# Kernel tuning notes

Measured on AMD Instinct MI355X. Metric: run time of the kernel, lower is better.

## Reference

```python
import jax, jax.numpy as jnp
import numpy as np

B1, B2, D = 8192, 8192, 128


def _cdist(d1, d2):
    # L2 distance matrix via the |a|^2 + |b|^2 - 2ab expansion (GEMM-dominant).
    d1_sq = jnp.sum(d1 * d1, axis=1, keepdims=True)          # (B1, 1)
    d2_sq = jnp.sum(d2 * d2, axis=1, keepdims=True)          # (B2, 1)
    dm = d1_sq + d2_sq.T - 2.0 * (d1 @ d2.T)                 # (B1, B2)
    return jnp.sqrt(jnp.clip(dm, 0.0))


def setup_inputs() -> dict:
    key = jax.random.key(0)
    k1, k2 = jax.random.split(key)
    desc1 = jax.random.normal(k1, (B1, D), dtype=jnp.float32)
    desc2 = jax.random.normal(k2, (B2, D), dtype=jnp.float32)
    return {"desc1": desc1, "desc2": desc2}


def reference(desc1, desc2):
    # DescriptorMatcher(match_mode='nn'): nearest neighbor in desc2 for each desc1.
    dm = _cdist(desc1, desc2)                                # (B1, B2)
    idxs_in_2 = jnp.argmin(dm, axis=1)                       # (B1,)
    match_dists = jnp.take_along_axis(dm, idxs_in_2[:, None], axis=1)  # (B1, 1)
    idxs_in_1 = jnp.arange(dm.shape[0], dtype=jnp.int64 if jax.config.jax_enable_x64 else jnp.int32)
    matches_idxs = jnp.stack([idxs_in_1, idxs_in_2.astype(idxs_in_1.dtype)], axis=1)  # (B1, 2)
    return match_dists, matches_idxs
```

## Files before the change

kernel.cpp:

```cpp
#include <hip/hip_runtime.h>
#include <cstdint>

#define NB1 8192
#define NB2 8192
#define DDIM 128
#define KROW 256
#define NSTEP 12

using half8   = __attribute__((ext_vector_type(8))) _Float16;
using half4   = __attribute__((ext_vector_type(4))) _Float16;
using float4v = __attribute__((ext_vector_type(4))) float;

typedef __attribute__((address_space(3))) void       lds_void;
typedef const __attribute__((address_space(1))) void glb_void;

__device__ inline unsigned long long packkey(float v, int j) {
  unsigned u = __float_as_uint(v);
  u = (u & 0x80000000u) ? ~u : (u | 0x80000000u);
  return ((unsigned long long)u << 32) | (unsigned)j;
}

__device__ __forceinline__ int a_src(int kt) { return (kt < 8) ? kt : kt - 8; }
__device__ __forceinline__ int b_src(int kt) { return (kt < 4) ? kt : kt - 4; }

__global__ __launch_bounds__(256) void convert_kernel(
    const float* __restrict__ d1, const float* __restrict__ d2,
    _Float16* __restrict__ A2, _Float16* __restrict__ B2,
    float* __restrict__ asq, float* __restrict__ bsq,
    unsigned long long* __restrict__ packed) {
  int gid  = blockIdx.x * 256 + threadIdx.x;
  int wv   = gid >> 6;
  int lane = gid & 63;
  int rowc = 2 * wv + (lane >> 5);
  bool isA = rowc < NB1;
  const float* src = isA ? d1 : d2;
  int row = isA ? rowc : rowc - NB1;
  int k4  = (lane & 31) * 4;

  float4 v = *(const float4*)&src[row * DDIM + k4];
  _Float16 h0 = (_Float16)v.x, h1 = (_Float16)v.y;
  _Float16 h2 = (_Float16)v.z, h3 = (_Float16)v.w;
  half4 hh = {h0, h1, h2, h3};
  half4 ll = {(_Float16)(v.x - (float)h0), (_Float16)(v.y - (float)h1),
              (_Float16)(v.z - (float)h2), (_Float16)(v.w - (float)h3)};

  _Float16* dst = (isA ? A2 : B2) + (size_t)row * KROW;
  *(half4*)&dst[k4]       = hh;
  *(half4*)&dst[128 + k4] = ll;

  float s = v.x * v.x + v.y * v.y + v.z * v.z + v.w * v.w;
  #pragma unroll
  for (int off = 16; off > 0; off >>= 1) s += __shfl_xor(s, off, 64);
  if ((lane & 31) == 0) (isA ? asq : bsq)[row] = s;

  if (gid < NB1) packed[gid] = 0xFFFFFFFFFFFFFFFFull;
}

__global__ __launch_bounds__(512, 2) void mfma_match_kernel(
    const _Float16* __restrict__ A2, const _Float16* __restrict__ B2,
    const float* __restrict__ bsq, unsigned long long* __restrict__ packed) {
  __shared__ unsigned long long smem[16384];
  _Float16* S = (_Float16*)smem;

  const int t    = threadIdx.x;
  const int lane = t & 63;
  const int wid  = t >> 6;
  const int wm   = wid >> 1;
  const int wn   = wid & 1;
  const int lx   = lane & 15, q = lane >> 4;

  const int id  = blockIdx.x;
  const int xcd = id & 7, kk = id >> 3;
  const int bx = (xcd & 1) * 16 + (kk & 15);
  const int by = (xcd >> 1) * 8 + (kk >> 4);
  const int row0 = bx * 256, col0 = by * 256;

  const int rstg  = t >> 2;
  const int cslot = t & 3;

  float4v acc[4][8];
  #pragma unroll
  for (int m = 0; m < 4; ++m)
    #pragma unroll
    for (int c = 0; c < 8; ++c) acc[m][c] = (float4v){0.f, 0.f, 0.f, 0.f};

  const int jc0 = col0 + wn * 128 + lx;
  float bq[8];
  #pragma unroll
  for (int c = 0; c < 8; ++c) bq[c] = bsq[jc0 + 16 * c];

  auto stage = [&](int kt, int buf) {
    const int koA = a_src(kt) * 32, koB = b_src(kt) * 32;
    #pragma unroll
    for (int call = 0; call < 2; ++call) {
      const int R  = call * 128 + rstg;
      const int cc = (cslot - (R >> 1)) & 3;
      const _Float16* ga = A2 + (size_t)(row0 + R) * KROW + koA + cc * 8;
      __builtin_amdgcn_global_load_lds((glb_void*)ga,
          (lds_void*)(S + buf * 16384 + call * 4096 + wid * 512), 16, 0, 0);
      const _Float16* gb = B2 + (size_t)(col0 + R) * KROW + koB + cc * 8;
      __builtin_amdgcn_global_load_lds((glb_void*)gb,
          (lds_void*)(S + buf * 16384 + 8192 + call * 4096 + wid * 512), 16, 0, 0);
    }
  };

  const int sw = ((q + (lx >> 1)) & 3) * 8;

  auto compute = [&](int buf) {
    const _Float16* Ab = S + buf * 16384;
    const _Float16* Bb = Ab + 8192;
    half8 af[4], bf[8];
    #pragma unroll
    for (int m = 0; m < 4; ++m)
      af[m] = *(const half8*)&Ab[(wm * 64 + 16 * m + lx) * 32 + sw];
    #pragma unroll
    for (int c = 0; c < 8; ++c)
      bf[c] = *(const half8*)&Bb[(wn * 128 + 16 * c + lx) * 32 + sw];
    __builtin_amdgcn_s_setprio(1);
    #pragma unroll
    for (int m = 0; m < 4; ++m)
      #pragma unroll
      for (int c = 0; c < 8; ++c)
        acc[m][c] = __builtin_amdgcn_mfma_f32_16x16x32_f16(
            af[m], bf[c], acc[m][c], 0, 0, 0);
    __builtin_amdgcn_s_setprio(0);
  };

  stage(0, 0); stage(1, 1); stage(2, 2);

#define STEP(K, N)                                                    \
  do {                                                                \
    asm volatile("s_waitcnt vmcnt(" #N ")" ::: "memory");             \
    __builtin_amdgcn_s_barrier();                                     \
    asm volatile("" ::: "memory");                                    \
    if constexpr ((K) + 3 < NSTEP) stage((K) + 3, ((K) + 3) & 3);     \
    compute((K) & 3);                                                 \
  } while (0)

  STEP(0, 8);  STEP(1, 8);  STEP(2, 8);  STEP(3, 8);
  STEP(4, 8);  STEP(5, 8);  STEP(6, 8);  STEP(7, 8);
  STEP(8, 8);  STEP(9, 8);  STEP(10, 4); STEP(11, 0);
#undef STEP

  __syncthreads();
  #pragma unroll
  for (int m = 0; m < 4; ++m) {
    #pragma unroll
    for (int reg = 0; reg < 4; ++reg) {
      float bv = 1e30f; int bj = 0;
      #pragma unroll
      for (int c = 0; c < 8; ++c) {
        float val = fmaf(-2.f, acc[m][c][reg], bq[c]);
        if (val < bv) { bv = val; bj = jc0 + 16 * c; }
      }
      const int mrow = wm * 64 + 16 * m + 4 * q + reg;
      smem[mrow * 33 + wn * 16 + lx] = packkey(bv, bj);
    }
  }
  __syncthreads();
  if (t < 256) {
    unsigned long long best = ~0ull;
    #pragma unroll
    for (int c = 0; c < 32; ++c) {
      unsigned long long kx = smem[t * 33 + ((2 * t + c) & 31)];
      if (kx < best) best = kx;
    }
    atomicMin(&packed[row0 + t], best);
  }
}

__global__ __launch_bounds__(256) void out_kernel(
    const unsigned long long* __restrict__ packed,
    const float* __restrict__ asq, float* __restrict__ out) {
  int r = blockIdx.x * 256 + threadIdx.x;
  unsigned long long best = packed[r];
  unsigned u = (unsigned)(best >> 32);
  u = (u & 0x80000000u) ? (u & 0x7fffffffu) : ~u;
  float val  = __uint_as_float(u);
  float dist = sqrtf(fmaxf(asq[r] + val, 0.f));
  int j = (int)(unsigned)(best & 0xffffffffu);
  out[r]               = dist;
  out[NB1 + 2 * r]     = (float)r;
  out[NB1 + 2 * r + 1] = (float)j;
}

extern "C" void kernel_launch(void* const* d_in, const int* in_sizes, int n_in,
                              void* d_out, int out_size, void* d_ws, size_t ws_size,
                              hipStream_t stream) {
  const float* d1 = (const float*)d_in[0];
  const float* d2 = (const float*)d_in[1];
  float* out = (float*)d_out;

  char* w = (char*)d_ws;
  float* asq = (float*)w;
  float* bsq = (float*)(w + 32768);
  _Float16* A2 = (_Float16*)(w + 65536);
  _Float16* B2 = (_Float16*)(w + 65536 + 4194304);
  unsigned long long* packed =
      (unsigned long long*)(w + 65536 + 2 * 4194304);

  convert_kernel<<<(NB1 + NB2) / 8, 256, 0, stream>>>(
      d1, d2, A2, B2, asq, bsq, packed);

  mfma_match_kernel<<<(NB1 / 256) * (NB2 / 256), 512, 0, stream>>>(
      A2, B2, bsq, packed);

  out_kernel<<<NB1 / 256, 256, 0, stream>>>(packed, asq, out);
}
```

Measured before the change: 117.8 us.

## Double-buffer LDS fragment reads into registers to overlap with MFMA

Splits the per-step compute into an LDS-read phase and an MFMA phase. It keeps two register sets of A/B fragments so the next K-step's fragments load while the current step's MFMAs run. The vmcnt waits are retuned to this one-step-ahead schedule. The bsq column-norm loads move to the epilogue to cut live registers during the main loop. A plain load now guards the atomicMin so rows that cannot improve skip the atomic. The extra fragment registers raise VGPR pressure under the 512x2 launch bound, which could cause spills or lower occupancy.

```diff
diff --git a/kernel.cpp b/kernel.cpp
--- a/kernel.cpp
+++ b/kernel.cpp
@@ -84,11 +84,6 @@
     #pragma unroll
     for (int c = 0; c < 8; ++c) acc[m][c] = (float4v){0.f, 0.f, 0.f, 0.f};
 
-  const int jc0 = col0 + wn * 128 + lx;
-  float bq[8];
-  #pragma unroll
-  for (int c = 0; c < 8; ++c) bq[c] = bsq[jc0 + 16 * c];
-
   auto stage = [&](int kt, int buf) {
     const int koA = a_src(kt) * 32, koB = b_src(kt) * 32;
     #pragma unroll
@@ -106,16 +101,18 @@
 
   const int sw = ((q + (lx >> 1)) & 3) * 8;
 
-  auto compute = [&](int buf) {
+  auto rd = [&](int buf, half8 (&af)[4], half8 (&bf)[8]) {
     const _Float16* Ab = S + buf * 16384;
     const _Float16* Bb = Ab + 8192;
-    half8 af[4], bf[8];
     #pragma unroll
     for (int m = 0; m < 4; ++m)
       af[m] = *(const half8*)&Ab[(wm * 64 + 16 * m + lx) * 32 + sw];
     #pragma unroll
     for (int c = 0; c < 8; ++c)
       bf[c] = *(const half8*)&Bb[(wn * 128 + 16 * c + lx) * 32 + sw];
+  };
+
+  auto mm = [&](half8 (&af)[4], half8 (&bf)[8]) {
     __builtin_amdgcn_s_setprio(1);
     #pragma unroll
     for (int m = 0; m < 4; ++m)
@@ -126,23 +123,44 @@
     __builtin_amdgcn_s_setprio(0);
   };
 
+  half8 afA[4], bfA[8], afB[4], bfB[8];
+
   stage(0, 0); stage(1, 1); stage(2, 2);
-
-#define STEP(K, N)                                                    \
+  asm volatile("s_waitcnt vmcnt(8)" ::: "memory");
+  __builtin_amdgcn_s_barrier();
+  asm volatile("" ::: "memory");
+  rd(0, afA, bfA);
+
+#define STEP(K, NV, MSET, RSET, DOST, DORD)                           \
   do {                                                                \
-    asm volatile("s_waitcnt vmcnt(" #N ")" ::: "memory");             \
+    asm volatile("s_waitcnt vmcnt(" #NV ")" ::: "memory");            \
     __builtin_amdgcn_s_barrier();                                     \
     asm volatile("" ::: "memory");                                    \
-    if constexpr ((K) + 3 < NSTEP) stage((K) + 3, ((K) + 3) & 3);     \
-    compute((K) & 3);                                                 \
+    if constexpr (DOST) stage((K) + 3, ((K) + 3) & 3);                \
+    if constexpr (DORD) rd(((K) + 1) & 3, af##RSET, bf##RSET);        \
+    mm(af##MSET, bf##MSET);                                           \
   } while (0)
 
-  STEP(0, 8);  STEP(1, 8);  STEP(2, 8);  STEP(3, 8);
-  STEP(4, 8);  STEP(5, 8);  STEP(6, 8);  STEP(7, 8);
-  STEP(8, 8);  STEP(9, 8);  STEP(10, 4); STEP(11, 0);
+  STEP(0, 4, A, B, true, true);
+  STEP(1, 4, B, A, true, true);
+  STEP(2, 4, A, B, true, true);
+  STEP(3, 4, B, A, true, true);
+  STEP(4, 4, A, B, true, true);
+  STEP(5, 4, B, A, true, true);
+  STEP(6, 4, A, B, true, true);
+  STEP(7, 4, B, A, true, true);
+  STEP(8, 4, A, B, true, true);
+  STEP(9, 4, B, A, false, true);
+  STEP(10, 0, A, B, false, true);
 #undef STEP
+  mm(afB, bfB);
 
   __syncthreads();
+  const int jc0 = col0 + wn * 128 + lx;
+  float bq[8];
+  #pragma unroll
+  for (int c = 0; c < 8; ++c) bq[c] = bsq[jc0 + 16 * c];
+
   #pragma unroll
   for (int m = 0; m < 4; ++m) {
     #pragma unroll
@@ -165,7 +183,8 @@
       unsigned long long kx = smem[t * 33 + ((2 * t + c) & 31)];
       if (kx < best) best = kx;
     }
-    atomicMin(&packed[row0 + t], best);
+    unsigned long long cur = packed[row0 + t];
+    if (best < cur) atomicMin(&packed[row0 + t], best);
   }
 }
 
```

After: 140.3 us. +19.1%, slower.

## Restructure MFMA match kernel into 2x4 wave grid with phased double-buffer pipeline

Applied to the files above, without the earlier changes.

The GEMM main loop is rebuilt. Waves now sit in a 2x4 grid, each owning a 128x64 output sub-tile instead of 64x128. Global-to-LDS staging moves from a 4-slot single-k-step ring to two 64KB buffers, each holding two k-slices, and each tile is split into four phases that interleave LDS reads, async prefetch and 16-MFMA batches with barriers between them. The epilogue adds a shuffle-based partial min, and the final atomicMin is skipped when the existing value is already smaller. The goal is better overlap of memory and compute and fewer LDS fragment reads per MFMA, at the cost of more barriers and more complex wait-count bookkeeping.

```diff
diff --git a/kernel.cpp b/kernel.cpp
--- a/kernel.cpp
+++ b/kernel.cpp
@@ -5,7 +5,6 @@
 #define NB2 8192
 #define DDIM 128
 #define KROW 256
-#define NSTEP 12
 
 using half8   = __attribute__((ext_vector_type(8))) _Float16;
 using half4   = __attribute__((ext_vector_type(4))) _Float16;
@@ -19,9 +18,6 @@
   u = (u & 0x80000000u) ? ~u : (u | 0x80000000u);
   return ((unsigned long long)u << 32) | (unsigned)j;
 }
-
-__device__ __forceinline__ int a_src(int kt) { return (kt < 8) ? kt : kt - 8; }
-__device__ __forceinline__ int b_src(int kt) { return (kt < 4) ? kt : kt - 4; }
 
 __global__ __launch_bounds__(256) void convert_kernel(
     const float* __restrict__ d1, const float* __restrict__ d2,
@@ -60,14 +56,16 @@
     const _Float16* __restrict__ A2, const _Float16* __restrict__ B2,
     const float* __restrict__ bsq, unsigned long long* __restrict__ packed) {
   __shared__ unsigned long long smem[16384];
-  _Float16* S = (_Float16*)smem;
+  _Float16* S  = (_Float16*)smem;
+  char*     Sb = (char*)smem;
 
   const int t    = threadIdx.x;
   const int lane = t & 63;
   const int wid  = t >> 6;
-  const int wm   = wid >> 1;
-  const int wn   = wid & 1;
+  const int wm   = wid >> 2;
+  const int wn   = wid & 3;
   const int lx   = lane & 15, q = lane >> 4;
+  const int sw   = ((q + (lx >> 1)) & 3) * 8;
 
   const int id  = blockIdx.x;
   const int xcd = id & 7, kk = id >> 3;
@@ -75,86 +73,129 @@
   const int by = (xcd >> 1) * 8 + (kk >> 4);
   const int row0 = bx * 256, col0 = by * 256;
 
-  const int rstg  = t >> 2;
-  const int cslot = t & 3;
-
-  float4v acc[4][8];
-  #pragma unroll
-  for (int m = 0; m < 4; ++m)
-    #pragma unroll
-    for (int c = 0; c < 8; ++c) acc[m][c] = (float4v){0.f, 0.f, 0.f, 0.f};
-
-  const int jc0 = col0 + wn * 128 + lx;
-  float bq[8];
-  #pragma unroll
-  for (int c = 0; c < 8; ++c) bq[c] = bsq[jc0 + 16 * c];
-
-  auto stage = [&](int kt, int buf) {
-    const int koA = a_src(kt) * 32, koB = b_src(kt) * 32;
-    #pragma unroll
-    for (int call = 0; call < 2; ++call) {
-      const int R  = call * 128 + rstg;
-      const int cc = (cslot - (R >> 1)) & 3;
-      const _Float16* ga = A2 + (size_t)(row0 + R) * KROW + koA + cc * 8;
-      __builtin_amdgcn_global_load_lds((glb_void*)ga,
-          (lds_void*)(S + buf * 16384 + call * 4096 + wid * 512), 16, 0, 0);
-      const _Float16* gb = B2 + (size_t)(col0 + R) * KROW + koB + cc * 8;
-      __builtin_amdgcn_global_load_lds((glb_void*)gb,
-          (lds_void*)(S + buf * 16384 + 8192 + call * 4096 + wid * 512), 16, 0, 0);
-    }
-  };
-
-  const int sw = ((q + (lx >> 1)) & 3) * 8;
-
-  auto compute = [&](int buf) {
-    const _Float16* Ab = S + buf * 16384;
-    const _Float16* Bb = Ab + 8192;
-    half8 af[4], bf[8];
-    #pragma unroll
-    for (int m = 0; m < 4; ++m)
-      af[m] = *(const half8*)&Ab[(wm * 64 + 16 * m + lx) * 32 + sw];
-    #pragma unroll
-    for (int c = 0; c < 8; ++c)
-      bf[c] = *(const half8*)&Bb[(wn * 128 + 16 * c + lx) * 32 + sw];
+  const int rp   = t >> 2;
+  const int s3   = t & 3;
+  const int qt   = (s3 - ((t >> 3) & 3)) & 3;
+  const int aRow = (rp & 63) + ((rp >> 6) << 7);
+
+  const _Float16* pA = A2 + (size_t)(row0 + aRow) * KROW + qt * 8;
+  const _Float16* pB = B2 + (size_t)(col0 + rp) * KROW + qt * 8;
+  const int dA = aRow * 64 + s3 * 16;
+  const int dB = rp * 64 + s3 * 16;
+
+  float4v acc[8][4];
+  #pragma unroll
+  for (int m = 0; m < 8; ++m)
+    #pragma unroll
+    for (int c = 0; c < 4; ++c) acc[m][c] = (float4v){0.f, 0.f, 0.f, 0.f};
+
+  auto stA = [&](int buf, int mh, int ks, int aK) {
+    __builtin_amdgcn_global_load_lds(
+        (glb_void*)(pA + mh * 16384 + aK * 32),
+        (lds_void*)(Sb + buf * 65536 + ks * 16384 + mh * 4096 + dA), 16, 0, 0);
+  };
+  auto stB = [&](int buf, int rh, int ks, int bK) {
+    __builtin_amdgcn_global_load_lds(
+        (glb_void*)(pB + rh * 32768 + bK * 32),
+        (lds_void*)(Sb + buf * 65536 + 32768 + ks * 16384 + rh * 8192 + dB),
+        16, 0, 0);
+  };
+
+  half8 af[4], bf[4];
+  auto rdA = [&](int buf, int mh, int ks) {
+    const _Float16* Ab =
+        S + buf * 32768 + ks * 8192 + (wm * 128 + mh * 64 + lx) * 32 + sw;
+    #pragma unroll
+    for (int r = 0; r < 4; ++r) af[r] = *(const half8*)&Ab[r * 512];
+  };
+  auto rdB = [&](int buf, int ks) {
+    const _Float16* Bb =
+        S + buf * 32768 + 16384 + ks * 8192 + (wn * 64 + lx) * 32 + sw;
+    #pragma unroll
+    for (int c = 0; c < 4; ++c) bf[c] = *(const half8*)&Bb[c * 512];
+  };
+  auto mfma16 = [&](int mh) {
     __builtin_amdgcn_s_setprio(1);
     #pragma unroll
-    for (int m = 0; m < 4; ++m)
+    for (int r = 0; r < 4; ++r)
       #pragma unroll
-      for (int c = 0; c < 8; ++c)
-        acc[m][c] = __builtin_amdgcn_mfma_f32_16x16x32_f16(
-            af[m], bf[c], acc[m][c], 0, 0, 0);
+      for (int c = 0; c < 4; ++c)
+        acc[mh * 4 + r][c] = __builtin_amdgcn_mfma_f32_16x16x32_f16(
+            af[r], bf[c], acc[mh * 4 + r][c], 0, 0, 0);
     __builtin_amdgcn_s_setprio(0);
   };
 
-  stage(0, 0); stage(1, 1); stage(2, 2);
-
-#define STEP(K, N)                                                    \
-  do {                                                                \
-    asm volatile("s_waitcnt vmcnt(" #N ")" ::: "memory");             \
-    __builtin_amdgcn_s_barrier();                                     \
-    asm volatile("" ::: "memory");                                    \
-    if constexpr ((K) + 3 < NSTEP) stage((K) + 3, ((K) + 3) & 3);     \
-    compute((K) & 3);                                                 \
-  } while (0)
-
-  STEP(0, 8);  STEP(1, 8);  STEP(2, 8);  STEP(3, 8);
-  STEP(4, 8);  STEP(5, 8);  STEP(6, 8);  STEP(7, 8);
-  STEP(8, 8);  STEP(9, 8);  STEP(10, 4); STEP(11, 0);
-#undef STEP
+#define BAR() do { __builtin_amdgcn_s_barrier(); \
+                   asm volatile("" ::: "memory"); } while (0)
+
+  stA(0, 0, 0, 0); stB(0, 0, 0, 0); stB(0, 1, 0, 0); stA(0, 1, 0, 0);
+  stA(0, 0, 1, 1); stB(0, 0, 1, 1); stB(0, 1, 1, 1); stA(0, 1, 1, 1);
+  asm volatile("s_waitcnt vmcnt(4)" ::: "memory");
+  BAR();
+
+#define PH0(BUF, NBUF, AK0, BK0, DOST)                                \
+  do { rdA(BUF, 0, 0); rdB(BUF, 0);                                   \
+       if constexpr (DOST) { stA(NBUF, 0, 0, AK0); stB(NBUF, 0, 0, BK0); } \
+       BAR(); mfma16(0); BAR(); } while (0)
+#define PH1(BUF, NBUF, AK0, BK0, DOST, VM)                            \
+  do { rdA(BUF, 1, 0);                                                \
+       if constexpr (DOST) { stB(NBUF, 1, 0, BK0); stA(NBUF, 1, 0, AK0); } \
+       BAR(); mfma16(1);                                              \
+       asm volatile("s_waitcnt vmcnt(" VM ")" ::: "memory");          \
+       BAR(); } while (0)
+#define PH2(BUF, NBUF, AK1, BK1, DOST)                                \
+  do { rdA(BUF, 0, 1); rdB(BUF, 1);                                   \
+       if constexpr (DOST) { stA(NBUF, 0, 1, AK1); stB(NBUF, 0, 1, BK1); } \
+       BAR(); mfma16(0); BAR(); } while (0)
+#define PH3(BUF, NBUF, AK1, BK1, DOST, DOVM)                          \
+  do { rdA(BUF, 1, 1);                                                \
+       if constexpr (DOST) { stB(NBUF, 1, 1, BK1); stA(NBUF, 1, 1, AK1); } \
+       BAR(); mfma16(1);                                              \
+       if constexpr (DOVM)                                            \
+         asm volatile("s_waitcnt vmcnt(4)" ::: "memory");             \
+       BAR(); } while (0)
+
+#define TILE(BUF, NBUF, AK0, AK1, BK0, BK1, DOST, VM1, DOVM3)         \
+  PH0(BUF, NBUF, AK0, BK0, DOST);                                     \
+  PH1(BUF, NBUF, AK0, BK0, DOST, VM1);                                \
+  PH2(BUF, NBUF, AK1, BK1, DOST);                                     \
+  PH3(BUF, NBUF, AK1, BK1, DOST, DOVM3)
+
+  TILE(0, 1, 2, 3, 2, 3, true, "4", true);
+  TILE(1, 0, 4, 5, 0, 1, true, "4", true);
+  TILE(0, 1, 6, 7, 2, 3, true, "4", true);
+  TILE(1, 0, 0, 1, 4, 5, true, "4", true);
+  TILE(0, 1, 2, 3, 6, 7, true, "4", true);
+  TILE(1, 0, 0, 0, 0, 0, false, "0", false);
+#undef TILE
+#undef PH0
+#undef PH1
+#undef PH2
+#undef PH3
 
   __syncthreads();
-  #pragma unroll
-  for (int m = 0; m < 4; ++m) {
+  const int jc0 = col0 + wn * 64 + lx;
+  float bq[4];
+  #pragma unroll
+  for (int c = 0; c < 4; ++c) bq[c] = bsq[jc0 + 16 * c];
+
+  #pragma unroll
+  for (int m = 0; m < 8; ++m) {
     #pragma unroll
     for (int reg = 0; reg < 4; ++reg) {
       float bv = 1e30f; int bj = 0;
       #pragma unroll
-      for (int c = 0; c < 8; ++c) {
+      for (int c = 0; c < 4; ++c) {
         float val = fmaf(-2.f, acc[m][c][reg], bq[c]);
         if (val < bv) { bv = val; bj = jc0 + 16 * c; }
       }
-      const int mrow = wm * 64 + 16 * m + 4 * q + reg;
-      smem[mrow * 33 + wn * 16 + lx] = packkey(bv, bj);
+      unsigned long long key = packkey(bv, bj);
+      unsigned long long oth = __shfl_xor(key, 8, 64);
+      if (oth < key) key = oth;
+      if ((lx & 8) == 0) {
+        const int mrow = wm * 128 + m * 16 + 4 * q + reg;
+        smem[mrow * 33 + wn * 8 + (lx & 7)] = key;
+      }
     }
   }
   __syncthreads();
@@ -162,10 +203,11 @@
     unsigned long long best = ~0ull;
     #pragma unroll
     for (int c = 0; c < 32; ++c) {
-      unsigned long long kx = smem[t * 33 + ((2 * t + c) & 31)];
+      unsigned long long kx = smem[t * 33 + ((t + c) & 31)];
       if (kx < best) best = kx;
     }
-    atomicMin(&packed[row0 + t], best);
+    unsigned long long cur = packed[row0 + t];
+    if (best < cur) atomicMin(&packed[row0 + t], best);
   }
 }
 
```

Result: slower. 129.1 us (+9.7%).

## Load A fragments directly to registers and stage only B through LDS

Applied to the files above, without the earlier changes.

The A operand now goes straight from global memory into double-buffered register fragments (afA/afB), one K step ahead. Only B is staged through LDS, in a 3-buffer ring instead of the 4-buffer A+B ring. This cuts shared memory from 128KB to about 66KB, which could let two 512-thread blocks fit per CU, and removes the LDS round trip for A. The cost is more VGPR pressure and less-coalesced, strided global loads for A that depend on cache hits. The row-min atomicMin is now skipped when the current stored value is already smaller, and the bsq loads move to after the main loop.

```diff
diff --git a/kernel.cpp b/kernel.cpp
--- a/kernel.cpp
+++ b/kernel.cpp
@@ -59,8 +59,8 @@
 __global__ __launch_bounds__(512, 2) void mfma_match_kernel(
     const _Float16* __restrict__ A2, const _Float16* __restrict__ B2,
     const float* __restrict__ bsq, unsigned long long* __restrict__ packed) {
-  __shared__ unsigned long long smem[16384];
-  _Float16* S = (_Float16*)smem;
+  __shared__ unsigned long long smem[8448];
+  _Float16* SB = (_Float16*)smem;
 
   const int t    = threadIdx.x;
   const int lane = t & 63;
@@ -77,6 +77,10 @@
 
   const int rstg  = t >> 2;
   const int cslot = t & 3;
+  const int cc    = (cslot - (rstg >> 1)) & 3;
+  const _Float16* gB0 = B2 + (size_t)(col0 + rstg) * KROW + cc * 8;
+
+  const _Float16* pAq = A2 + (size_t)(row0 + wm * 64 + lx) * KROW + q * 8;
 
   float4v acc[4][8];
   #pragma unroll
@@ -84,38 +88,32 @@
     #pragma unroll
     for (int c = 0; c < 8; ++c) acc[m][c] = (float4v){0.f, 0.f, 0.f, 0.f};
 
-  const int jc0 = col0 + wn * 128 + lx;
-  float bq[8];
-  #pragma unroll
-  for (int c = 0; c < 8; ++c) bq[c] = bsq[jc0 + 16 * c];
-
-  auto stage = [&](int kt, int buf) {
-    const int koA = a_src(kt) * 32, koB = b_src(kt) * 32;
-    #pragma unroll
-    for (int call = 0; call < 2; ++call) {
-      const int R  = call * 128 + rstg;
-      const int cc = (cslot - (R >> 1)) & 3;
-      const _Float16* ga = A2 + (size_t)(row0 + R) * KROW + koA + cc * 8;
-      __builtin_amdgcn_global_load_lds((glb_void*)ga,
-          (lds_void*)(S + buf * 16384 + call * 4096 + wid * 512), 16, 0, 0);
-      const _Float16* gb = B2 + (size_t)(col0 + R) * KROW + koB + cc * 8;
-      __builtin_amdgcn_global_load_lds((glb_void*)gb,
-          (lds_void*)(S + buf * 16384 + 8192 + call * 4096 + wid * 512), 16, 0, 0);
-    }
+  auto stageB = [&](int kt, int buf) {
+    const int ko = b_src(kt) * 32;
+    __builtin_amdgcn_global_load_lds((glb_void*)(gB0 + ko),
+        (lds_void*)(SB + buf * 8192 + wid * 512), 16, 0, 0);
+    __builtin_amdgcn_global_load_lds((glb_void*)(gB0 + 128 * KROW + ko),
+        (lds_void*)(SB + buf * 8192 + 4096 + wid * 512), 16, 0, 0);
+  };
+
+  half8 afA[4], afB[4], bf[8];
+
+  auto ldA = [&](int kt, half8 (&af)[4]) {
+    const int ko = a_src(kt) * 32;
+    #pragma unroll
+    for (int r = 0; r < 4; ++r)
+      af[r] = *(const half8*)&pAq[(size_t)(16 * r) * KROW + ko];
   };
 
   const int sw = ((q + (lx >> 1)) & 3) * 8;
-
-  auto compute = [&](int buf) {
-    const _Float16* Ab = S + buf * 16384;
-    const _Float16* Bb = Ab + 8192;
-    half8 af[4], bf[8];
-    #pragma unroll
-    for (int m = 0; m < 4; ++m)
-      af[m] = *(const half8*)&Ab[(wm * 64 + 16 * m + lx) * 32 + sw];
+  auto rdB = [&](int buf) {
+    const _Float16* Bb = SB + buf * 8192;
     #pragma unroll
     for (int c = 0; c < 8; ++c)
       bf[c] = *(const half8*)&Bb[(wn * 128 + 16 * c + lx) * 32 + sw];
+  };
+
+  auto mm = [&](half8 (&af)[4]) {
     __builtin_amdgcn_s_setprio(1);
     #pragma unroll
     for (int m = 0; m < 4; ++m)
@@ -126,23 +124,50 @@
     __builtin_amdgcn_s_setprio(0);
   };
 
-  stage(0, 0); stage(1, 1); stage(2, 2);
-
-#define STEP(K, N)                                                    \
+#define FENCE() asm volatile("" ::: "memory")
+
+  ldA(0, afA);
+  FENCE();
+  stageB(0, 0); stageB(1, 1);
+  asm volatile("s_waitcnt vmcnt(2)" ::: "memory");
+  __builtin_amdgcn_s_barrier();
+  FENCE();
+
+#define STEP(K, VM, MS, RS, DOA, DOB)                                 \
   do {                                                                \
-    asm volatile("s_waitcnt vmcnt(" #N ")" ::: "memory");             \
-    __builtin_amdgcn_s_barrier();                                     \
-    asm volatile("" ::: "memory");                                    \
-    if constexpr ((K) + 3 < NSTEP) stage((K) + 3, ((K) + 3) & 3);     \
-    compute((K) & 3);                                                 \
+    if constexpr ((K) > 0) {                                          \
+      asm volatile("s_waitcnt vmcnt(" VM ")" ::: "memory");           \
+      __builtin_amdgcn_s_barrier();                                   \
+      FENCE();                                                        \
+    }                                                                 \
+    if constexpr (DOA) ldA((K) + 1, af##RS);                          \
+    FENCE();                                                          \
+    if constexpr (DOB) stageB((K) + 2, ((K) + 2) % 3);                \
+    FENCE();                                                          \
+    rdB((K) % 3);                                                     \
+    mm(af##MS);                                                       \
   } while (0)
 
-  STEP(0, 8);  STEP(1, 8);  STEP(2, 8);  STEP(3, 8);
-  STEP(4, 8);  STEP(5, 8);  STEP(6, 8);  STEP(7, 8);
-  STEP(8, 8);  STEP(9, 8);  STEP(10, 4); STEP(11, 0);
+  STEP(0,  "2", A, B, true,  true);
+  STEP(1,  "2", B, A, true,  true);
+  STEP(2,  "2", A, B, true,  true);
+  STEP(3,  "2", B, A, true,  true);
+  STEP(4,  "2", A, B, true,  true);
+  STEP(5,  "2", B, A, true,  true);
+  STEP(6,  "2", A, B, true,  true);
+  STEP(7,  "2", B, A, true,  true);
+  STEP(8,  "2", A, B, true,  true);
+  STEP(9,  "2", B, A, true,  true);
+  STEP(10, "2", A, B, true,  false);
+  STEP(11, "0", B, A, false, false);
 #undef STEP
 
   __syncthreads();
+  const int jc0 = col0 + wn * 128 + lx;
+  float bq[8];
+  #pragma unroll
+  for (int c = 0; c < 8; ++c) bq[c] = bsq[jc0 + 16 * c];
+
   #pragma unroll
   for (int m = 0; m < 4; ++m) {
     #pragma unroll
@@ -165,7 +190,8 @@
       unsigned long long kx = smem[t * 33 + ((2 * t + c) & 31)];
       if (kx < best) best = kx;
     }
-    atomicMin(&packed[row0 + t], best);
+    unsigned long long cur = packed[row0 + t];
+    if (best < cur) atomicMin(&packed[row0 + t], best);
   }
 }
 
```

Measured after the change: 138.1 us. 1.17x slower.
